# Optimization experiments

Hardware: AMD Instinct MI355X
Metric: run time of the kernel (lower is better)

## Reference

```python
import jax, jax.numpy as jnp
import numpy as np


def batch_pairwise_dist(x, y):
    # x: [B, N, D], y: [B, M, D] -> P: [B, N, M] squared distances
    xx = jnp.sum(x * x, axis=-1)            # [B, N]
    yy = jnp.sum(y * y, axis=-1)            # [B, M]
    zz = jnp.einsum('bnd,bmd->bnm', x, y)   # [B, N, M]
    return xx[:, :, None] + yy[:, None, :] - 2.0 * zz


def setup_inputs() -> dict:
    key = jax.random.key(0)
    k1, k2 = jax.random.split(key)
    B, N, M, D = 8, 8192, 8192, 3
    preds = jax.random.normal(k1, (B, M, D), dtype=jnp.float32)
    gts = jax.random.normal(k2, (B, N, D), dtype=jnp.float32)
    return {"preds": preds, "gts": gts}


def reference(preds, gts):
    P = batch_pairwise_dist(gts, preds)     # [B, N, M]
    loss_1 = jnp.sum(jnp.min(P, axis=1))    # min over gts points
    loss_2 = jnp.sum(jnp.min(P, axis=2))    # min over preds points
    return loss_1 + loss_2
```

## Files before the change

kernel.cpp:

```cpp
#include <hip/hip_runtime.h>
#include <hip/hip_bf16.h>

#define BATCH 8
#define NPTS  8192
#define NPT_TOT (BATCH * NPTS)

typedef __attribute__((ext_vector_type(8)))  short short8;
typedef __attribute__((ext_vector_type(16))) float float16;
typedef unsigned int uint32;

__device__ __forceinline__ unsigned short bf16_of(float f) {
    __hip_bfloat16 h = __float2bfloat16(f);
    return *reinterpret_cast<unsigned short*>(&h);
}
__device__ __forceinline__ float f_of_bf16(unsigned short u) {
    __hip_bfloat16 h = *reinterpret_cast<__hip_bfloat16*>(&u);
    return __bfloat162float(h);
}
__device__ __forceinline__ uint32 pk(unsigned short lo, unsigned short hi) {
    return (uint32)lo | ((uint32)hi << 16);
}
__device__ __forceinline__ float max3f(float a, float b, float c) {
    float d;
    asm("v_max3_f32 %0, %1, %2, %3" : "=v"(d) : "v"(a), "v"(b), "v"(c));
    return d;
}

__global__ __launch_bounds__(256)
void prepass(const float* __restrict__ gts, const float* __restrict__ preds,
             float* __restrict__ norms,
             unsigned short* __restrict__ AG, unsigned short* __restrict__ BG,
             unsigned short* __restrict__ AP, unsigned short* __restrict__ BP)
{
    int i = blockIdx.x * blockDim.x + threadIdx.x;
    if (i >= 2 * NPT_TOT) return;
    const bool isGt = i < NPT_TOT;
    const int j = isGt ? i : i - NPT_TOT;
    const float* src = (isGt ? gts : preds) + 3 * (size_t)j;
    const float x = src[0], y = src[1], z = src[2];
    const float h = 0.5f * (x * x + y * y + z * z);
    norms[i] = h;

    const unsigned short xh = bf16_of(x), yh = bf16_of(y), zh = bf16_of(z);
    const unsigned short xl = bf16_of(x - f_of_bf16(xh));
    const unsigned short yl = bf16_of(y - f_of_bf16(yh));
    const unsigned short zl = bf16_of(z - f_of_bf16(zh));
    const unsigned short nhh = bf16_of(-h);
    const unsigned short nhl = bf16_of(-h - f_of_bf16(nhh));
    const unsigned short one = 0x3F80;

    unsigned short* A = (isGt ? AG : AP) + (size_t)j * 16;
    uint4 av0 = { pk(xh, yh), pk(zh, xl), pk(yl, zl), pk(xh, yh) };
    uint4 av1 = { pk(zh, xl), pk(yl, zl), pk(one, one), 0u };
    *reinterpret_cast<uint4*>(A)     = av0;
    *reinterpret_cast<uint4*>(A + 8) = av1;

    const int b = j >> 13;
    const int q = j & 8191;
    const int t = q >> 5, p = q & 31;
    unsigned short* Bf = (isGt ? BG : BP) + ((size_t)b * 16384 + t * 64 + p) * 8;
    uint4 bv0 = { pk(xh, yh), pk(zh, xh), pk(yh, zh), pk(xl, yl) };
    uint4 bv1 = { pk(zl, xl), pk(yl, zl), pk(nhh, nhl), 0u };
    *reinterpret_cast<uint4*>(Bf)            = bv0;
    *reinterpret_cast<uint4*>(Bf + 32 * 8)   = bv1;
}

#define MFMA_V(D, Asrc, Bsrc, Csrc)                                          \
    asm volatile("v_mfma_f32_32x32x16_bf16 %0, %1, %2, %3"                   \
                 : "=&v"(D) : "v"(Asrc), "v"(Bsrc), "v"(Csrc))

#define RED8(d, mx)                                   \
    {  mx = max3f(d[0],  d[1],  mx);                  \
       mx = max3f(d[2],  d[3],  mx);                  \
       mx = max3f(d[4],  d[5],  mx);                  \
       mx = max3f(d[6],  d[7],  mx);                  \
       mx = max3f(d[8],  d[9],  mx);                  \
       mx = max3f(d[10], d[11], mx);                  \
       mx = max3f(d[12], d[13], mx);                  \
       mx = max3f(d[14], d[15], mx); }

#define CT 16

__global__ __launch_bounds__(256, 4)
void chamfer_mfma(const unsigned short* __restrict__ AG,
                  const unsigned short* __restrict__ BP,
                  const unsigned short* __restrict__ AP,
                  const unsigned short* __restrict__ BG,
                  float* __restrict__ P)
{
    __shared__ short8 sb[CT * 64];

    const int tid   = threadIdx.x;
    const int lane  = tid & 63;
    const int wid   = tid >> 6;
    const int dir   = blockIdx.z >> 3;
    const int batch = blockIdx.z & 7;
    const int row0  = blockIdx.y * 256 + wid * 64;

    const unsigned short* Arows = dir ? AP : AG;
    const unsigned short* Bcols = dir ? BG : BP;

    const int lr = lane & 31, lg = lane >> 5;

    const short8* gB = reinterpret_cast<const short8*>(Bcols)
                     + (size_t)batch * 16384 + (size_t)blockIdx.x * (CT * 64);
#pragma unroll
    for (int s = 0; s < 4; ++s) sb[s * 256 + tid] = gB[s * 256 + tid];

    const short8* gA = reinterpret_cast<const short8*>(Arows);
    const size_t abase = ((size_t)batch * NPTS + row0 + lr) * 2 + lg;
    const short8 a0 = gA[abase];
    const short8 a1 = gA[abase + 64];

    float16 z16 = {0.f, 0.f, 0.f, 0.f, 0.f, 0.f, 0.f, 0.f,
                   0.f, 0.f, 0.f, 0.f, 0.f, 0.f, 0.f, 0.f};
    float mx0 = -INFINITY, mx1 = -INFINITY;

    __syncthreads();

    for (int tt = 0; tt < CT; ++tt) {
        const short8 bv = sb[tt * 64 + lane];

        float16 d;
        MFMA_V(d, bv, a0, z16);
        asm volatile("s_nop 7\n\ts_nop 7" : "+v"(d));
        RED8(d, mx0);

        MFMA_V(d, bv, a1, z16);
        asm volatile("s_nop 7\n\ts_nop 7" : "+v"(d));
        RED8(d, mx1);
    }

    mx0 = fmaxf(mx0, __shfl_xor(mx0, 32, 64));
    mx1 = fmaxf(mx1, __shfl_xor(mx1, 32, 64));
    if (lane < 32) {
        float* p = P + (((size_t)blockIdx.z * 16 + blockIdx.x) * NPTS) + row0 + lane;
        p[0]  = mx0;
        p[32] = mx1;
    }
}

__global__ __launch_bounds__(256)
void final_stage1(const float* __restrict__ norms, const float* __restrict__ P,
                  float* __restrict__ partials)
{
    const int base = blockIdx.x * 1024;
    float s = 0.f;
    for (int k = threadIdx.x; k < 1024; k += 256) {
        const int r = base + k;
        const int db  = r >> 13;
        const int row = r & 8191;
        const float* pp = P + ((size_t)db * 16) * NPTS + row;
        float m = pp[0];
#pragma unroll
        for (int c = 1; c < 16; ++c) m = fmaxf(m, pp[(size_t)c * NPTS]);
        s += norms[r] - m;
    }
#pragma unroll
    for (int off = 32; off; off >>= 1) s += __shfl_down(s, off, 64);
    __shared__ float ws4[4];
    if ((threadIdx.x & 63) == 0) ws4[threadIdx.x >> 6] = s;
    __syncthreads();
    if (threadIdx.x == 0) partials[blockIdx.x] = (ws4[0] + ws4[1]) + (ws4[2] + ws4[3]);
}

__global__ void final_stage2(const float* __restrict__ partials, float* __restrict__ out)
{
    float s = partials[threadIdx.x] + partials[threadIdx.x + 64];
#pragma unroll
    for (int off = 32; off; off >>= 1) s += __shfl_down(s, off, 64);
    if (threadIdx.x == 0) *out = 2.0f * s;
}

extern "C" void kernel_launch(void* const* d_in, const int* in_sizes, int n_in,
                              void* d_out, int out_size, void* d_ws, size_t ws_size,
                              hipStream_t stream) {
    const float* preds = (const float*)d_in[0];
    const float* gts   = (const float*)d_in[1];

    char* w = (char*)d_ws;
    float* norms = (float*)w;
    const size_t PITCH = 32 * (size_t)NPT_TOT;
    unsigned short* AG = (unsigned short*)(w + 8 * (size_t)NPT_TOT);
    unsigned short* BG = (unsigned short*)((char*)AG + PITCH);
    unsigned short* AP = (unsigned short*)((char*)AG + 2 * PITCH);
    unsigned short* BP = (unsigned short*)((char*)AG + 3 * PITCH);
    float* P        = (float*)((char*)AG + 4 * PITCH);
    float* partials = P + (size_t)16 * 16 * NPTS;

    prepass<<<(2 * NPT_TOT) / 256, 256, 0, stream>>>(gts, preds, norms,
                                                     AG, BG, AP, BP);

    dim3 grid(16, 32, 16);
    chamfer_mfma<<<grid, 256, 0, stream>>>(AG, BP, AP, BG, P);

    final_stage1<<<128, 256, 0, stream>>>(norms, P, partials);
    final_stage2<<<1, 64, 0, stream>>>(partials, (float*)d_out);
}
```

Baseline: 53.73 us.

## Transpose partial-max layout, unroll MFMA tile loop, widen final reduction grid

The chamfer kernel now preloads eight B fragments from LDS at a time and fully unrolls the 16-tile MFMA loop, so LDS reads can be hoisted ahead of the MFMAs. Partial maxima are stored row-major with 16 contiguous column-block values per row, which lets the reduction stage read each row with four float4 loads instead of 16 strided loads. The reduction grid grows from 128 to 512 blocks with one row per thread, and stage 2 sums 512 partials. The trade-offs are strided scalar stores from the MFMA kernel and higher register pressure from the unrolling.

```diff
diff --git a/kernel.cpp b/kernel.cpp
--- a/kernel.cpp
+++ b/kernel.cpp
@@ -79,6 +79,16 @@
        mx = max3f(d[12], d[13], mx);                  \
        mx = max3f(d[14], d[15], mx); }
 
+#define TILE(bv)                                                   \
+    {   float16 d;                                                 \
+        MFMA_V(d, bv, a0, z16);                                    \
+        asm volatile("s_nop 7\n\ts_nop 7" : "+v"(d));              \
+        RED8(d, mx0);                                              \
+        MFMA_V(d, bv, a1, z16);                                    \
+        asm volatile("s_nop 7\n\ts_nop 7" : "+v"(d));              \
+        RED8(d, mx1);                                              \
+    }
+
 #define CT 16
 
 __global__ __launch_bounds__(256, 4)
@@ -118,25 +128,37 @@
 
     __syncthreads();
 
-    for (int tt = 0; tt < CT; ++tt) {
-        const short8 bv = sb[tt * 64 + lane];
-
-        float16 d;
-        MFMA_V(d, bv, a0, z16);
-        asm volatile("s_nop 7\n\ts_nop 7" : "+v"(d));
-        RED8(d, mx0);
-
-        MFMA_V(d, bv, a1, z16);
-        asm volatile("s_nop 7\n\ts_nop 7" : "+v"(d));
-        RED8(d, mx1);
+    {
+        const short8 b0 = sb[0 * 64 + lane];
+        const short8 b1 = sb[1 * 64 + lane];
+        const short8 b2 = sb[2 * 64 + lane];
+        const short8 b3 = sb[3 * 64 + lane];
+        const short8 b4 = sb[4 * 64 + lane];
+        const short8 b5 = sb[5 * 64 + lane];
+        const short8 b6 = sb[6 * 64 + lane];
+        const short8 b7 = sb[7 * 64 + lane];
+        TILE(b0); TILE(b1); TILE(b2); TILE(b3);
+        TILE(b4); TILE(b5); TILE(b6); TILE(b7);
+    }
+    {
+        const short8 b0 = sb[8  * 64 + lane];
+        const short8 b1 = sb[9  * 64 + lane];
+        const short8 b2 = sb[10 * 64 + lane];
+        const short8 b3 = sb[11 * 64 + lane];
+        const short8 b4 = sb[12 * 64 + lane];
+        const short8 b5 = sb[13 * 64 + lane];
+        const short8 b6 = sb[14 * 64 + lane];
+        const short8 b7 = sb[15 * 64 + lane];
+        TILE(b0); TILE(b1); TILE(b2); TILE(b3);
+        TILE(b4); TILE(b5); TILE(b6); TILE(b7);
     }
 
     mx0 = fmaxf(mx0, __shfl_xor(mx0, 32, 64));
     mx1 = fmaxf(mx1, __shfl_xor(mx1, 32, 64));
     if (lane < 32) {
-        float* p = P + (((size_t)blockIdx.z * 16 + blockIdx.x) * NPTS) + row0 + lane;
-        p[0]  = mx0;
-        p[32] = mx1;
+        float* p = P + ((size_t)(blockIdx.z * NPTS + row0 + lane)) * 16 + blockIdx.x;
+        p[0]        = mx0;
+        p[32 * 16]  = mx1;
     }
 }
 
@@ -144,18 +166,18 @@
 void final_stage1(const float* __restrict__ norms, const float* __restrict__ P,
                   float* __restrict__ partials)
 {
-    const int base = blockIdx.x * 1024;
-    float s = 0.f;
-    for (int k = threadIdx.x; k < 1024; k += 256) {
-        const int r = base + k;
-        const int db  = r >> 13;
-        const int row = r & 8191;
-        const float* pp = P + ((size_t)db * 16) * NPTS + row;
-        float m = pp[0];
-#pragma unroll
-        for (int c = 1; c < 16; ++c) m = fmaxf(m, pp[(size_t)c * NPTS]);
-        s += norms[r] - m;
-    }
+    const int r = blockIdx.x * 256 + threadIdx.x;
+    const float4* pp = reinterpret_cast<const float4*>(P + (size_t)r * 16);
+    const float4 v0 = pp[0], v1 = pp[1], v2 = pp[2], v3 = pp[3];
+    float m = max3f(v0.x, v0.y, fmaxf(v0.z, v0.w));
+    m = max3f(v1.x, v1.y, m);
+    m = max3f(v1.z, v1.w, m);
+    m = max3f(v2.x, v2.y, m);
+    m = max3f(v2.z, v2.w, m);
+    m = max3f(v3.x, v3.y, m);
+    m = max3f(v3.z, v3.w, m);
+    float s = norms[r] - m;
+
 #pragma unroll
     for (int off = 32; off; off >>= 1) s += __shfl_down(s, off, 64);
     __shared__ float ws4[4];
@@ -166,7 +188,9 @@
 
 __global__ void final_stage2(const float* __restrict__ partials, float* __restrict__ out)
 {
-    float s = partials[threadIdx.x] + partials[threadIdx.x + 64];
+    float s = 0.f;
+#pragma unroll
+    for (int k = 0; k < 8; ++k) s += partials[threadIdx.x + 64 * k];
 #pragma unroll
     for (int off = 32; off; off >>= 1) s += __shfl_down(s, off, 64);
     if (threadIdx.x == 0) *out = 2.0f * s;
@@ -194,6 +218,6 @@
     dim3 grid(16, 32, 16);
     chamfer_mfma<<<grid, 256, 0, stream>>>(AG, BP, AP, BG, P);
 
-    final_stage1<<<128, 256, 0, stream>>>(norms, P, partials);
+    final_stage1<<<512, 256, 0, stream>>>(norms, P, partials);
     final_stage2<<<1, 64, 0, stream>>>(partials, (float*)d_out);
 }
```

After: 53.05 us. About the same (-1.3%).
